# Optimization experiments

Measured on AMD Instinct MI355X. Metric: run time of the kernel, lower is better.

The kernel has to match this reference:

```python
import math
import jax, jax.numpy as jnp
import numpy as np

N_HEADS, INPUT_DIM, EMBED_DIM = 8, 512, 512
KEY_DIM = EMBED_DIM // N_HEADS  # 64, val_dim == key_dim
BATCH, N = 4, 2048


def setup_inputs() -> dict:
    key = jax.random.key(0)
    ks = jax.random.split(key, 6)
    def unif(k, shape):
        stdv = 1.0 / math.sqrt(shape[-1])
        return jax.random.uniform(k, shape, jnp.float32, -stdv, stdv)
    q = jax.random.normal(ks[0], (BATCH, N, INPUT_DIM), jnp.float32)
    mask = jax.random.randint(ks[1], (BATCH, N, N), 0, 2, jnp.int32)
    W_query = unif(ks[2], (N_HEADS, INPUT_DIM, KEY_DIM))
    W_key = unif(ks[3], (N_HEADS, INPUT_DIM, KEY_DIM))
    W_val = unif(ks[4], (N_HEADS, INPUT_DIM, KEY_DIM))
    W_out = unif(ks[5], (N_HEADS, KEY_DIM, EMBED_DIM))
    return {"q": q, "mask": mask, "W_query": W_query, "W_key": W_key,
            "W_val": W_val, "W_out": W_out}


def reference(q, mask, W_query, W_key, W_val, W_out):
    # Self-attention: k is None, v is None -> k = q, v = q (module forward_).
    norm = 1.0 / math.sqrt(KEY_DIM)
    m = mask.astype(bool)[None]  # (1, b, nq, ng) broadcast over heads
    Q = jnp.einsum('bnd,hdk->hbnk', q, W_query)  # (h, b, nq, dk)
    K = jnp.einsum('bnd,hdk->hbnk', q, W_key)    # (h, b, ng, dk)
    V = jnp.einsum('bnd,hdv->hbnv', q, W_val)    # (h, b, ng, dv)
    scores = norm * jnp.einsum('hbqk,hbgk->hbqg', Q, K)  # (h, b, nq, ng)
    scores = jnp.where(m, -jnp.inf, scores)
    attn = jax.nn.softmax(scores, axis=-1)
    attn = jnp.where(m, 0.0, attn)  # zero out masked (also kills NaN rows)
    heads = jnp.einsum('hbqg,hbgv->hbqv', attn, V)
    out = jnp.einsum('hbqv,hve->bqe', heads, W_out)  # (b, nq, embed)
    return out
```

## Files before the change

### kernel.cpp

```cpp
#include <hip/hip_runtime.h>
#include <hip/hip_bf16.h>
#include <stdint.h>

using bf16 = __hip_bfloat16;
typedef __attribute__((ext_vector_type(8))) short short8;
typedef __attribute__((ext_vector_type(4))) short short4b;
typedef __attribute__((ext_vector_type(4))) float f32x4;
typedef __attribute__((ext_vector_type(4))) unsigned int u32x4;

#if __has_builtin(__builtin_amdgcn_exp2f)
#define EXP2(x) __builtin_amdgcn_exp2f(x)
#else
#define EXP2(x) exp2f(x)
#endif

__device__ __forceinline__ short8 load8(const bf16* p) {
  return *reinterpret_cast<const short8*>(p);
}
__device__ __forceinline__ short4b load4(const bf16* p) {
  return *reinterpret_cast<const short4b*>(p);
}
__device__ __forceinline__ short f2b(float f) {
  return __builtin_bit_cast(short, __float2bfloat16(f));
}
__device__ __forceinline__ unsigned int pk2(float a, float b) {
  return (unsigned int)(unsigned short)f2b(a) |
         ((unsigned int)(unsigned short)f2b(b) << 16);
}
__device__ __forceinline__ void asy16(const bf16* g, bf16* l) {
  __builtin_amdgcn_global_load_lds(
      (const __attribute__((address_space(1))) void*)g,
      (__attribute__((address_space(3))) void*)l, 16, 0, 0);
}


__global__ void k_xconv(const float4* __restrict__ x, ushort4* __restrict__ xb) {
  int i = blockIdx.x * 256 + threadIdx.x;
  float4 v = x[i];
  ushort4 o;
  o.x = (unsigned short)__builtin_bit_cast(short, __float2bfloat16(v.x));
  o.y = (unsigned short)__builtin_bit_cast(short, __float2bfloat16(v.y));
  o.z = (unsigned short)__builtin_bit_cast(short, __float2bfloat16(v.z));
  o.w = (unsigned short)__builtin_bit_cast(short, __float2bfloat16(v.w));
  xb[i] = o;
}

__global__ void k_maskpack(const int4* __restrict__ m4,
                           unsigned long long* __restrict__ bits) {
  int i = blockIdx.x * 256 + threadIdx.x;
  int4 v = m4[i];
  unsigned int nib = (unsigned)(v.x != 0) | ((unsigned)(v.y != 0) << 1) |
                     ((unsigned)(v.z != 0) << 2) | ((unsigned)(v.w != 0) << 3);
  unsigned long long w = (unsigned long long)nib << (4 * (threadIdx.x & 15));
  w |= __shfl_xor(w, 1);
  w |= __shfl_xor(w, 2);
  w |= __shfl_xor(w, 4);
  w |= __shfl_xor(w, 8);
  if ((threadIdx.x & 15) == 0) bits[i >> 4] = w;
}

__global__ void k_wprep(const float* __restrict__ Wq, const float* __restrict__ Wk,
                        const float* __restrict__ Wv, const float* __restrict__ Wo,
                        bf16* __restrict__ Wcat, bf16* __restrict__ Wot) {
  int t = blockIdx.x * 256 + threadIdx.x;
  if (t < 786432) {
    int rr = t >> 9, d = t & 511;
    int which = rr >> 9;
    int hdk = rr & 511, h = hdk >> 6, dk = hdk & 63;
    const float* W = (which == 0) ? Wq : ((which == 1) ? Wk : Wv);
    float v = W[(h * 512 + d) * 64 + dk];
    if (which == 0) v *= 0.18033688011112042f;
    Wcat[t] = __float2bfloat16(v);
  } else {
    int u = t - 786432;
    int e = u >> 9, hv = u & 511;
    Wot[u] = __float2bfloat16(Wo[hv * 512 + e]);
  }
}

__device__ __forceinline__ void gemm128(const bf16* __restrict__ A,
                                        const bf16* __restrict__ Bt,
                                        bf16* As, bf16* Bs,
                                        int rowBase, int colBase,
                                        f32x4 acc[4][4]) {
  const int tid = threadIdx.x;
  const int lane = tid & 63, w = tid >> 6;
  const int g = lane >> 4, r = lane & 15;

  auto stage = [&](int buf, int s) {
#pragma unroll
    for (int p = 0; p < 4; ++p) {
      int c = p * 256 + tid;
      int row = c >> 3, w8 = c & 7, sg = w8 ^ (row & 7);
      asy16(A + (size_t)(rowBase + row) * 512 + s * 64 + sg * 8,
            As + buf * 8192 + c * 8);
    }
#pragma unroll
    for (int p = 0; p < 4; ++p) {
      int c = p * 256 + tid;
      int row = c >> 3, w8 = c & 7, sg = w8 ^ (row & 7);
      asy16(Bt + (size_t)(colBase + row) * 512 + s * 64 + sg * 8,
            Bs + buf * 8192 + c * 8);
    }
  };

  stage(0, 0);
  int buf = 0;
  const int rbl = (w >> 1) * 64, cbl = (w & 1) * 64;
  for (int s = 0; s < 8; ++s) {
    __syncthreads();
    if (s < 7) stage(buf ^ 1, s + 1);
    const bf16* a0 = As + buf * 8192;
    const bf16* b0 = Bs + buf * 8192;
#pragma unroll
    for (int kk = 0; kk < 2; ++kk) {
      short8 af[4], bfr[4];
#pragma unroll
      for (int mt = 0; mt < 4; ++mt) {
        int row = rbl + mt * 16 + r;
        af[mt] = load8(a0 + (row * 8 + ((kk * 4 + g) ^ (row & 7))) * 8);
      }
#pragma unroll
      for (int nt = 0; nt < 4; ++nt) {
        int col = cbl + nt * 16 + r;
        bfr[nt] = load8(b0 + (col * 8 + ((kk * 4 + g) ^ (col & 7))) * 8);
      }
#pragma unroll
      for (int mt = 0; mt < 4; ++mt)
#pragma unroll
        for (int nt = 0; nt < 4; ++nt)
          acc[mt][nt] = __builtin_amdgcn_mfma_f32_16x16x32_bf16(
              af[mt], bfr[nt], acc[mt][nt], 0, 0, 0);
    }
    buf ^= 1;
  }
}

__global__ __launch_bounds__(256, 2) void k_proj_qkv(
    const bf16* __restrict__ Xb, const bf16* __restrict__ Wcat,
    bf16* __restrict__ Qb, bf16* __restrict__ Kb, bf16* __restrict__ Vt) {
  __shared__ __align__(16) bf16 As[2 * 8192];
  __shared__ __align__(16) bf16 Bs[2 * 8192];
  int rowBase = blockIdx.x * 128, colBase = blockIdx.y * 128;
  f32x4 acc[4][4] = {};
  gemm128(Xb, Wcat, As, Bs, rowBase, colBase, acc);
  const int lane = threadIdx.x & 63, w = threadIdx.x >> 6;
  const int g = lane >> 4, r = lane & 15;
#pragma unroll
  for (int mt = 0; mt < 4; ++mt) {
    int row0 = rowBase + (w >> 1) * 64 + mt * 16 + 4 * g;
    int b = row0 >> 11, n0 = row0 & 2047;
#pragma unroll
    for (int nt = 0; nt < 4; ++nt) {
      int col = colBase + (w & 1) * 64 + nt * 16 + r;
      if (col < 1024) {
        bf16* dst = (col < 512) ? Qb : Kb;
        int hh = (col >> 6) & 7, dk = col & 63;
        bf16* p0 = dst + ((size_t)(b * 8 + hh) * 2048 + n0) * 64 + dk;
#pragma unroll
        for (int rr = 0; rr < 4; ++rr)
          p0[rr * 64] = __float2bfloat16(acc[mt][nt][rr]);
      } else {
        int hdv = col - 1024;
        short4b pkv;
#pragma unroll
        for (int rr = 0; rr < 4; ++rr) pkv[rr] = f2b(acc[mt][nt][rr]);
        *reinterpret_cast<short4b*>(Vt + ((size_t)b * 512 + hdv) * 2048 + n0) = pkv;
      }
    }
  }
}

__global__ __launch_bounds__(256, 2) void k_proj_out(
    const bf16* __restrict__ O, const bf16* __restrict__ Wot,
    float* __restrict__ out) {
  __shared__ __align__(16) bf16 As[2 * 8192];
  __shared__ __align__(16) bf16 Bs[2 * 8192];
  int rowBase = blockIdx.x * 128, colBase = blockIdx.y * 128;
  f32x4 acc[4][4] = {};
  gemm128(O, Wot, As, Bs, rowBase, colBase, acc);
  const int lane = threadIdx.x & 63, w = threadIdx.x >> 6;
  const int g = lane >> 4, r = lane & 15;
#pragma unroll
  for (int mt = 0; mt < 4; ++mt) {
    int row0 = rowBase + (w >> 1) * 64 + mt * 16 + 4 * g;
#pragma unroll
    for (int nt = 0; nt < 4; ++nt) {
      int col = colBase + (w & 1) * 64 + nt * 16 + r;
#pragma unroll
      for (int rr = 0; rr < 4; ++rr)
        out[(size_t)(row0 + rr) * 512 + col] = acc[mt][nt][rr];
    }
  }
}

__global__ __launch_bounds__(256, 2) void k_attn(const bf16* __restrict__ Q,
    const bf16* __restrict__ K, const bf16* __restrict__ Vt,
    const unsigned long long* __restrict__ MB, bf16* __restrict__ O) {
  const int blin = blockIdx.x;
  const int j = blin >> 3;
  const int bh = (blin & 7) * 4 + (j >> 4);
  const int qt = j & 15;
  const int b = bh >> 3, h = bh & 7;
  const int tid = threadIdx.x;
  const int lane = tid & 63;
  const int wave = tid >> 6;
  const int g = lane >> 4, r = lane & 15;
  const int rx = r & 7;
  const int qbase = qt * 128 + wave * 32;

  __shared__ __align__(16) bf16 Kl[2][64 * 64];
  __shared__ __align__(16) bf16 Vl[2][64 * 64];

  const bf16* Kp = K + (size_t)bh * 2048 * 64;
  const bf16* Vp = Vt + (size_t)bh * 64 * 2048;

  short8 qf[2][2];
#pragma unroll
  for (int s = 0; s < 2; ++s) {
    const bf16* Qp = Q + ((size_t)bh * 2048 + qbase + s * 16 + r) * 64;
    qf[s][0] = load8(Qp + g * 8);
    qf[s][1] = load8(Qp + 32 + g * 8);
  }
  const unsigned long long* Mp0 = MB + ((size_t)b * 2048 + qbase + r) * 32;
  const unsigned long long* Mp1 = MB + ((size_t)b * 2048 + qbase + 16 + r) * 32;

  float l_part[2] = {0.f, 0.f};
  f32x4 acc[2][4] = {};

  auto stage = [&](int buf, int kt) {
    const bf16* Kg = Kp + kt * 4096;
    const bf16* Vg = Vp + kt * 64;
#pragma unroll
    for (int p = 0; p < 2; ++p) {
      int c = p * 256 + tid;
      int row = c >> 3, gr = c & 7, sg = gr ^ (row & 7);
      asy16(Kg + row * 64 + sg * 8, &Kl[buf][0] + c * 8);
    }
#pragma unroll
    for (int p = 0; p < 2; ++p) {
      int c = p * 256 + tid;
      int row = c >> 3, gr = c & 7, sg = gr ^ (row & 7);
      asy16(Vg + (size_t)row * 2048 + sg * 8, &Vl[buf][0] + c * 8);
    }
  };

  stage(0, 0);
  int buf = 0;

  for (int kt = 0; kt < 32; ++kt) {
    __syncthreads();
    if (kt < 31) stage(buf ^ 1, kt + 1);

    unsigned long long mw0 = Mp0[kt];
    unsigned long long mw1 = Mp1[kt];
    const bf16* kl = &Kl[buf][0];
    const bf16* vl = &Vl[buf][0];

    f32x4 st[4][2];
#pragma unroll
    for (int kc = 0; kc < 4; ++kc) {
      const bf16* krow = kl + (kc * 16 + r) * 64;
      short8 kf0 = load8(krow + ((g) ^ rx) * 8);
      short8 kf1 = load8(krow + ((4 + g) ^ rx) * 8);
      f32x4 z0 = {};
      z0 = __builtin_amdgcn_mfma_f32_16x16x32_bf16(kf0, qf[0][0], z0, 0, 0, 0);
      st[kc][0] = __builtin_amdgcn_mfma_f32_16x16x32_bf16(kf1, qf[0][1], z0, 0, 0, 0);
      f32x4 z1 = {};
      z1 = __builtin_amdgcn_mfma_f32_16x16x32_bf16(kf0, qf[1][0], z1, 0, 0, 0);
      st[kc][1] = __builtin_amdgcn_mfma_f32_16x16x32_bf16(kf1, qf[1][1], z1, 0, 0, 0);
    }

    short8 pa[2][2];
#pragma unroll
    for (int s = 0; s < 2; ++s) {
      unsigned long long mw = s ? mw1 : mw0;
      unsigned ml = (unsigned)mw >> (4 * g);
      unsigned mh = (unsigned)(mw >> 32) >> (4 * g);
      float p[16];
#pragma unroll
      for (int kc = 0; kc < 4; ++kc)
#pragma unroll
        for (int rr = 0; rr < 4; ++rr) {
          float e = EXP2(st[kc][s][rr]);
          unsigned wsel = (kc & 2) ? mh : ml;
          bool bad = (wsel >> (((kc & 1) << 4) + rr)) & 1u;
          p[kc * 4 + rr] = bad ? 0.f : e;
        }
      float s0 = (p[0] + p[1]) + (p[2] + p[3]);
      float s1 = (p[4] + p[5]) + (p[6] + p[7]);
      float s2 = (p[8] + p[9]) + (p[10] + p[11]);
      float s3 = (p[12] + p[13]) + (p[14] + p[15]);
      l_part[s] += (s0 + s1) + (s2 + s3);
      u32x4 q0, q1;
#pragma unroll
      for (int i2 = 0; i2 < 4; ++i2) {
        q0[i2] = pk2(p[2 * i2], p[2 * i2 + 1]);
        q1[i2] = pk2(p[8 + 2 * i2], p[8 + 2 * i2 + 1]);
      }
      pa[s][0] = __builtin_bit_cast(short8, q0);
      pa[s][1] = __builtin_bit_cast(short8, q1);
    }

#pragma unroll
    for (int dvs = 0; dvs < 4; ++dvs) {
      const bf16* vrow = vl + (dvs * 16 + r) * 64 + (g & 1) * 4;
      short4b v0 = load4(vrow + (((g >> 1)) ^ rx) * 8);
      short4b v1 = load4(vrow + ((2 + (g >> 1)) ^ rx) * 8);
      short4b v2 = load4(vrow + ((4 + (g >> 1)) ^ rx) * 8);
      short4b v3 = load4(vrow + ((6 + (g >> 1)) ^ rx) * 8);
      short8 vb0 = {v0[0], v0[1], v0[2], v0[3], v1[0], v1[1], v1[2], v1[3]};
      short8 vb1 = {v2[0], v2[1], v2[2], v2[3], v3[0], v3[1], v3[2], v3[3]};
#pragma unroll
      for (int s = 0; s < 2; ++s) {
        acc[s][dvs] = __builtin_amdgcn_mfma_f32_16x16x32_bf16(pa[s][0], vb0, acc[s][dvs], 0, 0, 0);
        acc[s][dvs] = __builtin_amdgcn_mfma_f32_16x16x32_bf16(pa[s][1], vb1, acc[s][dvs], 0, 0, 0);
      }
    }
    buf ^= 1;
  }

#pragma unroll
  for (int s = 0; s < 2; ++s) {
    float l = l_part[s];
    l += __shfl_xor(l, 16);
    l += __shfl_xor(l, 32);
    float l0 = __shfl(l, 4 * g + 0);
    float l1 = __shfl(l, 4 * g + 1);
    float l2 = __shfl(l, 4 * g + 2);
    float l3 = __shfl(l, 4 * g + 3);
    float i0 = (l0 > 0.f) ? 1.f / l0 : 0.f;
    float i1 = (l1 > 0.f) ? 1.f / l1 : 0.f;
    float i2 = (l2 > 0.f) ? 1.f / l2 : 0.f;
    float i3 = (l3 > 0.f) ? 1.f / l3 : 0.f;
    bf16* Op = O + ((size_t)b * 2048 + qbase + s * 16 + 4 * g) * 512 + h * 64;
#pragma unroll
    for (int dvs = 0; dvs < 4; ++dvs) {
      Op[0 * 512 + dvs * 16 + r] = __float2bfloat16(acc[s][dvs][0] * i0);
      Op[1 * 512 + dvs * 16 + r] = __float2bfloat16(acc[s][dvs][1] * i1);
      Op[2 * 512 + dvs * 16 + r] = __float2bfloat16(acc[s][dvs][2] * i2);
      Op[3 * 512 + dvs * 16 + r] = __float2bfloat16(acc[s][dvs][3] * i3);
    }
  }
}


extern "C" void kernel_launch(void* const* d_in, const int* in_sizes, int n_in,
                              void* d_out, int out_size, void* d_ws, size_t ws_size,
                              hipStream_t stream) {
  const float* q    = (const float*)d_in[0];
  const int*   mask = (const int*)d_in[1];
  const float* Wq   = (const float*)d_in[2];
  const float* Wk   = (const float*)d_in[3];
  const float* Wv   = (const float*)d_in[4];
  const float* Wo   = (const float*)d_in[5];
  float* out = (float*)d_out;

  char* ws = (char*)d_ws;
  const size_t MB1 = 1024 * 1024;
  bf16* Xb   = (bf16*)(ws + 0);
  bf16* Qb   = (bf16*)(ws + 8 * MB1);
  bf16* Kb   = (bf16*)(ws + 16 * MB1);
  bf16* Vtb  = (bf16*)(ws + 24 * MB1);
  bf16* Ob   = (bf16*)(ws + 32 * MB1);
  unsigned long long* Mbits = (unsigned long long*)(ws + 40 * MB1);
  bf16* Wcat = (bf16*)(ws + 42 * MB1);
  bf16* Wot  = (bf16*)(ws + 42 * MB1 + 1536 * 512 * 2);

  k_xconv<<<4096, 256, 0, stream>>>((const float4*)q, (ushort4*)Xb);
  k_maskpack<<<16384, 256, 0, stream>>>((const int4*)mask, Mbits);
  k_wprep<<<4096, 256, 0, stream>>>(Wq, Wk, Wv, Wo, Wcat, Wot);
  k_proj_qkv<<<dim3(64, 12), 256, 0, stream>>>(Xb, Wcat, Qb, Kb, Vtb);
  k_attn<<<512, 256, 0, stream>>>(Qb, Kb, Vtb, Mbits, Ob);
  k_proj_out<<<dim3(64, 4), 256, 0, stream>>>(Ob, Wot, out);
}
```

Before: 224.8 us.

## Halve attention query tile, sum softmax rows via MFMA, merge prep kernels

The attention kernel now gives each wave 16 query rows instead of 32. This doubles the grid to 1024 blocks and raises the launch-bounds occupancy hint to 4. The softmax row sum is computed by an MFMA against a vector of ones, which replaces the scalar adds and the cross-lane shuffles. The three preprocessing kernels (input convert, weight prep, mask packing) are merged into one launch. The cost is that K/V tiles are reused across half as many queries, so LDS and global traffic per unit of work doubles. The row sum is also taken from bf16-rounded probabilities.

```diff
diff --git a/kernel.cpp b/kernel.cpp
--- a/kernel.cpp
+++ b/kernel.cpp
@@ -33,48 +33,48 @@
       (__attribute__((address_space(3))) void*)l, 16, 0, 0);
 }
 
-
-__global__ void k_xconv(const float4* __restrict__ x, ushort4* __restrict__ xb) {
-  int i = blockIdx.x * 256 + threadIdx.x;
-  float4 v = x[i];
-  ushort4 o;
-  o.x = (unsigned short)__builtin_bit_cast(short, __float2bfloat16(v.x));
-  o.y = (unsigned short)__builtin_bit_cast(short, __float2bfloat16(v.y));
-  o.z = (unsigned short)__builtin_bit_cast(short, __float2bfloat16(v.z));
-  o.w = (unsigned short)__builtin_bit_cast(short, __float2bfloat16(v.w));
-  xb[i] = o;
-}
-
-__global__ void k_maskpack(const int4* __restrict__ m4,
-                           unsigned long long* __restrict__ bits) {
-  int i = blockIdx.x * 256 + threadIdx.x;
-  int4 v = m4[i];
-  unsigned int nib = (unsigned)(v.x != 0) | ((unsigned)(v.y != 0) << 1) |
-                     ((unsigned)(v.z != 0) << 2) | ((unsigned)(v.w != 0) << 3);
-  unsigned long long w = (unsigned long long)nib << (4 * (threadIdx.x & 15));
-  w |= __shfl_xor(w, 1);
-  w |= __shfl_xor(w, 2);
-  w |= __shfl_xor(w, 4);
-  w |= __shfl_xor(w, 8);
-  if ((threadIdx.x & 15) == 0) bits[i >> 4] = w;
-}
-
-__global__ void k_wprep(const float* __restrict__ Wq, const float* __restrict__ Wk,
-                        const float* __restrict__ Wv, const float* __restrict__ Wo,
-                        bf16* __restrict__ Wcat, bf16* __restrict__ Wot) {
-  int t = blockIdx.x * 256 + threadIdx.x;
-  if (t < 786432) {
-    int rr = t >> 9, d = t & 511;
-    int which = rr >> 9;
-    int hdk = rr & 511, h = hdk >> 6, dk = hdk & 63;
-    const float* W = (which == 0) ? Wq : ((which == 1) ? Wk : Wv);
-    float v = W[(h * 512 + d) * 64 + dk];
-    if (which == 0) v *= 0.18033688011112042f;
-    Wcat[t] = __float2bfloat16(v);
+__global__ void k_prep(const float4* __restrict__ x, ushort4* __restrict__ xb,
+                       const float* __restrict__ Wq, const float* __restrict__ Wk,
+                       const float* __restrict__ Wv, const float* __restrict__ Wo,
+                       bf16* __restrict__ Wcat, bf16* __restrict__ Wot,
+                       const int4* __restrict__ m4,
+                       unsigned long long* __restrict__ bits) {
+  int blk = blockIdx.x;
+  if (blk < 4096) {
+    int i = blk * 256 + threadIdx.x;
+    float4 v = x[i];
+    ushort4 o;
+    o.x = (unsigned short)f2b(v.x);
+    o.y = (unsigned short)f2b(v.y);
+    o.z = (unsigned short)f2b(v.z);
+    o.w = (unsigned short)f2b(v.w);
+    xb[i] = o;
+  } else if (blk < 8192) {
+    int t = (blk - 4096) * 256 + threadIdx.x;
+    if (t < 786432) {
+      int rr = t >> 9, d = t & 511;
+      int which = rr >> 9;
+      int hdk = rr & 511, h = hdk >> 6, dk = hdk & 63;
+      const float* W = (which == 0) ? Wq : ((which == 1) ? Wk : Wv);
+      float v = W[(h * 512 + d) * 64 + dk];
+      if (which == 0) v *= 0.18033688011112042f;
+      Wcat[t] = __float2bfloat16(v);
+    } else {
+      int u = t - 786432;
+      int e = u >> 9, hv = u & 511;
+      Wot[u] = __float2bfloat16(Wo[hv * 512 + e]);
+    }
   } else {
-    int u = t - 786432;
-    int e = u >> 9, hv = u & 511;
-    Wot[u] = __float2bfloat16(Wo[hv * 512 + e]);
+    int i = (blk - 8192) * 256 + threadIdx.x;
+    int4 v = m4[i];
+    unsigned int nib = (unsigned)(v.x != 0) | ((unsigned)(v.y != 0) << 1) |
+                       ((unsigned)(v.z != 0) << 2) | ((unsigned)(v.w != 0) << 3);
+    unsigned long long w = (unsigned long long)nib << (4 * (threadIdx.x & 15));
+    w |= __shfl_xor(w, 1);
+    w |= __shfl_xor(w, 2);
+    w |= __shfl_xor(w, 4);
+    w |= __shfl_xor(w, 8);
+    if ((threadIdx.x & 15) == 0) bits[i >> 4] = w;
   }
 }
 
@@ -194,20 +194,20 @@
   }
 }
 
-__global__ __launch_bounds__(256, 2) void k_attn(const bf16* __restrict__ Q,
+__global__ __launch_bounds__(256, 4) void k_attn(const bf16* __restrict__ Q,
     const bf16* __restrict__ K, const bf16* __restrict__ Vt,
     const unsigned long long* __restrict__ MB, bf16* __restrict__ O) {
   const int blin = blockIdx.x;
   const int j = blin >> 3;
-  const int bh = (blin & 7) * 4 + (j >> 4);
-  const int qt = j & 15;
+  const int bh = (blin & 7) * 4 + (j >> 5);
+  const int qt = j & 31;
   const int b = bh >> 3, h = bh & 7;
   const int tid = threadIdx.x;
   const int lane = tid & 63;
   const int wave = tid >> 6;
   const int g = lane >> 4, r = lane & 15;
   const int rx = r & 7;
-  const int qbase = qt * 128 + wave * 32;
+  const int qbase = qt * 64 + wave * 16;
 
   __shared__ __align__(16) bf16 Kl[2][64 * 64];
   __shared__ __align__(16) bf16 Vl[2][64 * 64];
@@ -215,18 +215,17 @@
   const bf16* Kp = K + (size_t)bh * 2048 * 64;
   const bf16* Vp = Vt + (size_t)bh * 64 * 2048;
 
-  short8 qf[2][2];
-#pragma unroll
-  for (int s = 0; s < 2; ++s) {
-    const bf16* Qp = Q + ((size_t)bh * 2048 + qbase + s * 16 + r) * 64;
-    qf[s][0] = load8(Qp + g * 8);
-    qf[s][1] = load8(Qp + 32 + g * 8);
-  }
-  const unsigned long long* Mp0 = MB + ((size_t)b * 2048 + qbase + r) * 32;
-  const unsigned long long* Mp1 = MB + ((size_t)b * 2048 + qbase + 16 + r) * 32;
-
-  float l_part[2] = {0.f, 0.f};
-  f32x4 acc[2][4] = {};
+  const bf16* Qp = Q + ((size_t)bh * 2048 + qbase + r) * 64;
+  short8 qf0 = load8(Qp + g * 8);
+  short8 qf1 = load8(Qp + 32 + g * 8);
+  const unsigned long long* Mp = MB + ((size_t)b * 2048 + qbase + r) * 32;
+
+  short8 ones;
+#pragma unroll
+  for (int i = 0; i < 8; ++i) ones[i] = (short)0x3F80;
+
+  f32x4 acc[4] = {};
+  f32x4 acc_l = {};
 
   auto stage = [&](int buf, int kt) {
     const bf16* Kg = Kp + kt * 4096;
@@ -252,55 +251,44 @@
     __syncthreads();
     if (kt < 31) stage(buf ^ 1, kt + 1);
 
-    unsigned long long mw0 = Mp0[kt];
-    unsigned long long mw1 = Mp1[kt];
+    unsigned long long mw = Mp[kt];
     const bf16* kl = &Kl[buf][0];
     const bf16* vl = &Vl[buf][0];
 
-    f32x4 st[4][2];
+    f32x4 st[4];
 #pragma unroll
     for (int kc = 0; kc < 4; ++kc) {
       const bf16* krow = kl + (kc * 16 + r) * 64;
       short8 kf0 = load8(krow + ((g) ^ rx) * 8);
       short8 kf1 = load8(krow + ((4 + g) ^ rx) * 8);
-      f32x4 z0 = {};
-      z0 = __builtin_amdgcn_mfma_f32_16x16x32_bf16(kf0, qf[0][0], z0, 0, 0, 0);
-      st[kc][0] = __builtin_amdgcn_mfma_f32_16x16x32_bf16(kf1, qf[0][1], z0, 0, 0, 0);
-      f32x4 z1 = {};
-      z1 = __builtin_amdgcn_mfma_f32_16x16x32_bf16(kf0, qf[1][0], z1, 0, 0, 0);
-      st[kc][1] = __builtin_amdgcn_mfma_f32_16x16x32_bf16(kf1, qf[1][1], z1, 0, 0, 0);
-    }
-
-    short8 pa[2][2];
-#pragma unroll
-    for (int s = 0; s < 2; ++s) {
-      unsigned long long mw = s ? mw1 : mw0;
-      unsigned ml = (unsigned)mw >> (4 * g);
-      unsigned mh = (unsigned)(mw >> 32) >> (4 * g);
-      float p[16];
-#pragma unroll
-      for (int kc = 0; kc < 4; ++kc)
-#pragma unroll
-        for (int rr = 0; rr < 4; ++rr) {
-          float e = EXP2(st[kc][s][rr]);
-          unsigned wsel = (kc & 2) ? mh : ml;
-          bool bad = (wsel >> (((kc & 1) << 4) + rr)) & 1u;
-          p[kc * 4 + rr] = bad ? 0.f : e;
-        }
-      float s0 = (p[0] + p[1]) + (p[2] + p[3]);
-      float s1 = (p[4] + p[5]) + (p[6] + p[7]);
-      float s2 = (p[8] + p[9]) + (p[10] + p[11]);
-      float s3 = (p[12] + p[13]) + (p[14] + p[15]);
-      l_part[s] += (s0 + s1) + (s2 + s3);
-      u32x4 q0, q1;
-#pragma unroll
-      for (int i2 = 0; i2 < 4; ++i2) {
-        q0[i2] = pk2(p[2 * i2], p[2 * i2 + 1]);
-        q1[i2] = pk2(p[8 + 2 * i2], p[8 + 2 * i2 + 1]);
+      f32x4 z = {};
+      z = __builtin_amdgcn_mfma_f32_16x16x32_bf16(kf0, qf0, z, 0, 0, 0);
+      st[kc] = __builtin_amdgcn_mfma_f32_16x16x32_bf16(kf1, qf1, z, 0, 0, 0);
+    }
+
+    unsigned ml = (unsigned)mw >> (4 * g);
+    unsigned mh = (unsigned)(mw >> 32) >> (4 * g);
+    float p[16];
+#pragma unroll
+    for (int kc = 0; kc < 4; ++kc)
+#pragma unroll
+      for (int rr = 0; rr < 4; ++rr) {
+        float e = EXP2(st[kc][rr]);
+        unsigned wsel = (kc & 2) ? mh : ml;
+        bool bad = (wsel >> (((kc & 1) << 4) + rr)) & 1u;
+        p[kc * 4 + rr] = bad ? 0.f : e;
       }
-      pa[s][0] = __builtin_bit_cast(short8, q0);
-      pa[s][1] = __builtin_bit_cast(short8, q1);
-    }
+    u32x4 q0, q1;
+#pragma unroll
+    for (int i2 = 0; i2 < 4; ++i2) {
+      q0[i2] = pk2(p[2 * i2], p[2 * i2 + 1]);
+      q1[i2] = pk2(p[8 + 2 * i2], p[8 + 2 * i2 + 1]);
+    }
+    short8 pa0 = __builtin_bit_cast(short8, q0);
+    short8 pa1 = __builtin_bit_cast(short8, q1);
+
+    acc_l = __builtin_amdgcn_mfma_f32_16x16x32_bf16(pa0, ones, acc_l, 0, 0, 0);
+    acc_l = __builtin_amdgcn_mfma_f32_16x16x32_bf16(pa1, ones, acc_l, 0, 0, 0);
 
 #pragma unroll
     for (int dvs = 0; dvs < 4; ++dvs) {
@@ -311,37 +299,22 @@
       short4b v3 = load4(vrow + ((6 + (g >> 1)) ^ rx) * 8);
       short8 vb0 = {v0[0], v0[1], v0[2], v0[3], v1[0], v1[1], v1[2], v1[3]};
       short8 vb1 = {v2[0], v2[1], v2[2], v2[3], v3[0], v3[1], v3[2], v3[3]};
-#pragma unroll
-      for (int s = 0; s < 2; ++s) {
-        acc[s][dvs] = __builtin_amdgcn_mfma_f32_16x16x32_bf16(pa[s][0], vb0, acc[s][dvs], 0, 0, 0);
-        acc[s][dvs] = __builtin_amdgcn_mfma_f32_16x16x32_bf16(pa[s][1], vb1, acc[s][dvs], 0, 0, 0);
-      }
+      acc[dvs] = __builtin_amdgcn_mfma_f32_16x16x32_bf16(pa0, vb0, acc[dvs], 0, 0, 0);
+      acc[dvs] = __builtin_amdgcn_mfma_f32_16x16x32_bf16(pa1, vb1, acc[dvs], 0, 0, 0);
     }
     buf ^= 1;
   }
 
-#pragma unroll
-  for (int s = 0; s < 2; ++s) {
-    float l = l_part[s];
-    l += __shfl_xor(l, 16);
-    l += __shfl_xor(l, 32);
-    float l0 = __shfl(l, 4 * g + 0);
-    float l1 = __shfl(l, 4 * g + 1);
-    float l2 = __shfl(l, 4 * g + 2);
-    float l3 = __shfl(l, 4 * g + 3);
-    float i0 = (l0 > 0.f) ? 1.f / l0 : 0.f;
-    float i1 = (l1 > 0.f) ? 1.f / l1 : 0.f;
-    float i2 = (l2 > 0.f) ? 1.f / l2 : 0.f;
-    float i3 = (l3 > 0.f) ? 1.f / l3 : 0.f;
-    bf16* Op = O + ((size_t)b * 2048 + qbase + s * 16 + 4 * g) * 512 + h * 64;
-#pragma unroll
-    for (int dvs = 0; dvs < 4; ++dvs) {
-      Op[0 * 512 + dvs * 16 + r] = __float2bfloat16(acc[s][dvs][0] * i0);
-      Op[1 * 512 + dvs * 16 + r] = __float2bfloat16(acc[s][dvs][1] * i1);
-      Op[2 * 512 + dvs * 16 + r] = __float2bfloat16(acc[s][dvs][2] * i2);
-      Op[3 * 512 + dvs * 16 + r] = __float2bfloat16(acc[s][dvs][3] * i3);
-    }
-  }
+  float inv[4];
+#pragma unroll
+  for (int rr = 0; rr < 4; ++rr)
+    inv[rr] = (acc_l[rr] > 0.f) ? 1.f / acc_l[rr] : 0.f;
+  bf16* Op = O + ((size_t)b * 2048 + qbase + 4 * g) * 512 + h * 64;
+#pragma unroll
+  for (int dvs = 0; dvs < 4; ++dvs)
+#pragma unroll
+    for (int rr = 0; rr < 4; ++rr)
+      Op[rr * 512 + dvs * 16 + r] = __float2bfloat16(acc[dvs][rr] * inv[rr]);
 }
 
 
@@ -367,10 +340,10 @@
   bf16* Wcat = (bf16*)(ws + 42 * MB1);
   bf16* Wot  = (bf16*)(ws + 42 * MB1 + 1536 * 512 * 2);
 
-  k_xconv<<<4096, 256, 0, stream>>>((const float4*)q, (ushort4*)Xb);
-  k_maskpack<<<16384, 256, 0, stream>>>((const int4*)mask, Mbits);
-  k_wprep<<<4096, 256, 0, stream>>>(Wq, Wk, Wv, Wo, Wcat, Wot);
+  k_prep<<<24576, 256, 0, stream>>>((const float4*)q, (ushort4*)Xb,
+                                    Wq, Wk, Wv, Wo, Wcat, Wot,
+                                    (const int4*)mask, Mbits);
   k_proj_qkv<<<dim3(64, 12), 256, 0, stream>>>(Xb, Wcat, Qb, Kb, Vtb);
-  k_attn<<<512, 256, 0, stream>>>(Qb, Kb, Vtb, Mbits, Ob);
+  k_attn<<<1024, 256, 0, stream>>>(Qb, Kb, Vtb, Mbits, Ob);
   k_proj_out<<<dim3(64, 4), 256, 0, stream>>>(Ob, Wot, out);
 }
```

Result: no change. 223.7 us (-0.5%).
